# Performance work log

Measured on AMD Instinct MI355X. Metric: run time of the kernel, lower is better.

The kernel has to match this reference:

```python
import jax, jax.numpy as jnp
import numpy as np

BS, P, R, D = 32, 128, 16, 1024
RHO = 0.97
EPS = 1e-8


def unit_normalize(x):
    return x / jnp.maximum(jnp.linalg.norm(x, axis=-1, keepdims=True), EPS)


def setup_inputs() -> dict:
    key = jax.random.key(0)
    ks = jax.random.split(key, 12)
    scale = 1.0 / np.sqrt(D)
    return {
        "x_all": jax.random.normal(ks[0], (BS, P, D), jnp.float32),
        "h_all": jax.random.normal(ks[1], (BS, P, D), jnp.float32),
        "surprise_all": jax.random.uniform(ks[2], (BS, P, 1), jnp.float32) * 8.0,
        "reset_mask": jax.random.bernoulli(ks[3], 0.05, (BS, P)),
        "pm_K": unit_normalize(jax.random.normal(ks[4], (BS, R, D), jnp.float32)),
        "pm_V": unit_normalize(jax.random.normal(ks[5], (BS, R, D), jnp.float32)),
        "pm_a": jax.random.uniform(ks[6], (BS, R), jnp.float32),
        "elig_K0": jnp.zeros((BS, R, D), jnp.float32),
        "elig_V0": jnp.zeros((BS, R, D), jnp.float32),
        "W_k": jax.random.normal(ks[7], (D, D), jnp.float32) * scale,
        "b_k": jnp.zeros((D,), jnp.float32),
        "W_v": jax.random.normal(ks[8], (D, D), jnp.float32) * scale,
        "b_v": jnp.zeros((D,), jnp.float32),
    }


def reference(x_all, h_all, surprise_all, reset_mask, pm_K, pm_V, pm_a,
              elig_K0, elig_V0, W_k, b_k, W_v, b_v):
    # ---- apply_batch: read-only slot-memory readout over P tokens ----
    x_q = unit_normalize(x_all)                                  # [BS,P,D]
    scores = jnp.einsum('brd,bpd->bpr', pm_K, x_q)               # [BS,P,R]
    weighted = pm_a[:, None, :] * scores                         # [BS,P,R]
    y_pm = jnp.einsum('bpr,brd->bpd', weighted, pm_V)            # [BS,P,D]

    # ---- update_eligibility_batch: affine scan over P tokens ----
    k_cand = unit_normalize(jnp.einsum('bpd,de->bpe', x_all, W_k) + b_k)  # [BS,P,D]
    v_cand = jnp.einsum('bpd,de->bpe', h_all, W_v) + b_v                  # [BS,P,D]
    gate = jnp.clip(surprise_all[..., 0] / 5.0, 0.0, 1.0)                 # [BS,P]
    a_keep = RHO * (1.0 - reset_mask.astype(jnp.float32))                 # [BS,P]

    def step(carry, inp):
        eK, eV = carry                      # each [BS,R,D]
        k, v, g, a = inp                    # [BS,D],[BS,D],[BS],[BS]
        # b_t = gate * cand, broadcast across the R slots (matches torch expand)
        eK = a[:, None, None] * eK + (g[:, None] * k)[:, None, :]
        eV = a[:, None, None] * eV + (g[:, None] * v)[:, None, :]
        return (eK, eV), None

    xs = (jnp.swapaxes(k_cand, 0, 1), jnp.swapaxes(v_cand, 0, 1),
          gate.T, a_keep.T)                 # leading axis = P
    (elig_K, elig_V), _ = jax.lax.scan(step, (elig_K0, elig_V0), xs)

    return y_pm, elig_K, elig_V
```

## Files before the change

### kernel.cpp

```cpp
#include <hip/hip_runtime.h>
#include <cstdint>
#include <cstddef>

#define NB 32
#define NP 128
#define NR 16
#define ND 1024
#define RHOC 0.97f
#define EPSN 1e-8f

typedef short bf16x8 __attribute__((ext_vector_type(8)));
typedef float f32x4 __attribute__((ext_vector_type(4)));
typedef unsigned short u16x8 __attribute__((ext_vector_type(8)));
typedef unsigned short ushort_t;

__device__ inline ushort_t f2bf(float f) {
  unsigned u = __float_as_uint(f);
  unsigned r = (u + 0x7fffu + ((u >> 16) & 1u)) >> 16;
  return (ushort_t)r;
}
__device__ inline float bf2f(ushort_t v) {
  return __uint_as_float(((unsigned)v) << 16);
}
__device__ inline void gload16(const void* g, void* l) {
  __builtin_amdgcn_global_load_lds(
      (const __attribute__((address_space(1))) void*)g,
      (__attribute__((address_space(3))) void*)l, 16, 0, 0);
}

__global__ __launch_bounds__(256) void prep_kernel(
    const float* __restrict__ surprise, const void* __restrict__ mask,
    const float* __restrict__ x, const float* __restrict__ Wk,
    const float* __restrict__ pmK, const float* __restrict__ h,
    float* __restrict__ c, float* __restrict__ Abuf, float* __restrict__ csum,
    ushort_t* __restrict__ Xb, float* __restrict__ xnorm,
    ushort_t* __restrict__ WkT, ushort_t* __restrict__ pmKb,
    float* __restrict__ hbar) {
  __shared__ __align__(16) char smem[8448];
  int bid = blockIdx.x;
  int t = threadIdx.x;
  const unsigned char* mb = (const unsigned char*)mask;
  if (bid < NB) {
    float* a_sh = (float*)smem;
    float* suf  = a_sh + 128;
    float* redc = suf + 132;
    int*   isu8 = (int*)(redc + 128);
    int b = bid;
    if (t == 0) *isu8 = 0;
    __syncthreads();
    int v = 0;
    for (int i = t; i < NB * NP; i += 256)
      if ((i & 3) != 0 && mb[i] != 0) v = 1;
    if (v) *isu8 = 1;
    __syncthreads();
    int u8 = *isu8;
    if (t < NP) {
      int mv = u8 ? mb[b * NP + t] : ((const int*)mask)[b * NP + t];
      a_sh[t] = RHOC * (mv ? 0.f : 1.f);
    }
    __syncthreads();
    if (t == 0) {
      float p = 1.f;
      suf[NP] = 1.f;
      for (int s = NP - 1; s >= 0; --s) { p *= a_sh[s]; suf[s] = p; }
    }
    __syncthreads();
    if (t < NP) {
      float g = fminf(fmaxf(surprise[b * NP + t] * 0.2f, 0.f), 1.f);
      float cv = g * suf[t + 1];
      c[b * NP + t] = cv;
      redc[t] = cv;
    }
    __syncthreads();
    for (int off = 64; off > 0; off >>= 1) {
      if (t < off) redc[t] += redc[t + off];
      __syncthreads();
    }
    if (t == 0) { csum[b] = redc[0]; Abuf[b] = suf[0]; }
  } else if (bid < NB + 512) {
    int id = bid - NB;
    int b = id >> 4, dchunk = id & 15;
    float* asw = (float*)smem;
    float* suf = asw + 128;
    float* cs  = suf + 132;
    float* red = cs + 128;
    int* isu8  = (int*)(red + 256);
    if (t == 0) *isu8 = 0;
    __syncthreads();
    int v = 0;
    for (int i = t; i < NB * NP; i += 256)
      if ((i & 3) != 0 && mb[i] != 0) v = 1;
    if (v) *isu8 = 1;
    __syncthreads();
    int u8 = *isu8;
    if (t < NP) {
      int mv = u8 ? mb[b * NP + t] : ((const int*)mask)[b * NP + t];
      asw[t] = RHOC * (mv ? 0.f : 1.f);
    }
    __syncthreads();
    if (t == 0) {
      float p = 1.f;
      suf[NP] = 1.f;
      for (int s = NP - 1; s >= 0; --s) { p *= asw[s]; suf[s] = p; }
    }
    __syncthreads();
    if (t < NP) {
      float g = fminf(fmaxf(surprise[b * NP + t] * 0.2f, 0.f), 1.f);
      cs[t] = g * suf[t + 1];
    }
    __syncthreads();
    int dd = t & 63, sl = t >> 6;
    int d = dchunk * 64 + dd;
    const float* hb = h + ((size_t)b * NP + sl * 32) * ND + d;
    float acc = 0.f;
#pragma unroll
    for (int tt2 = 0; tt2 < 32; ++tt2)
      acc += cs[sl * 32 + tt2] * hb[(size_t)tt2 * ND];
    red[sl * 64 + dd] = acc;
    __syncthreads();
    if (sl == 0)
      hbar[(size_t)b * ND + d] = red[dd] + red[64 + dd] + red[128 + dd] + red[192 + dd];
  } else if (bid < NB + 512 + NB * NP) {
    int row = bid - (NB + 512);
    float* red = (float*)smem;
    float4 vv = *(const float4*)&x[(size_t)row * ND + t * 4];
    ushort4 o;
    o.x = f2bf(vv.x); o.y = f2bf(vv.y); o.z = f2bf(vv.z); o.w = f2bf(vv.w);
    *(ushort4*)&Xb[(size_t)row * ND + t * 4] = o;
    float ss = vv.x * vv.x + vv.y * vv.y + vv.z * vv.z + vv.w * vv.w;
#pragma unroll
    for (int off = 32; off > 0; off >>= 1) ss += __shfl_xor(ss, off);
    int wave = t >> 6, lane = t & 63;
    if (lane == 0) red[wave] = ss;
    __syncthreads();
    if (t == 0) xnorm[row] = sqrtf(red[0] + red[1] + red[2] + red[3]);
  } else if (bid < NB + 512 + NB * NP + 256) {
    int id2 = bid - (NB + 512 + NB * NP);
    ushort_t (*tt)[65] = (ushort_t(*)[65])smem;
    int k0 = (id2 >> 4) * 64, n0 = (id2 & 15) * 64;
#pragma unroll
    for (int i = 0; i < 16; ++i) {
      int r = i * 4 + (t >> 6), cc = t & 63;
      tt[r][cc] = f2bf(Wk[(size_t)(k0 + r) * ND + n0 + cc]);
    }
    __syncthreads();
#pragma unroll
    for (int i = 0; i < 16; ++i) {
      int r = i * 4 + (t >> 6), cc = t & 63;
      WkT[(size_t)(n0 + r) * ND + k0 + cc] = tt[cc][r];
    }
  } else {
    int id3 = bid - (NB + 512 + NB * NP + 256);
    size_t base = (size_t)id3 * 2048 + t * 8;
    float4 a = *(const float4*)&pmK[base];
    float4 bq = *(const float4*)&pmK[base + 4];
    u16x8 o;
    o[0] = f2bf(a.x); o[1] = f2bf(a.y); o[2] = f2bf(a.z); o[3] = f2bf(a.w);
    o[4] = f2bf(bq.x); o[5] = f2bf(bq.y); o[6] = f2bf(bq.z); o[7] = f2bf(bq.w);
    *(u16x8*)&pmKb[base] = o;
  }
}

__global__ __launch_bounds__(256, 3) void main_kernel(
    const ushort_t* __restrict__ Xb, const ushort_t* __restrict__ WkT,
    const float* __restrict__ bk, float* __restrict__ norms2p,
    const ushort_t* __restrict__ pmKb, const float* __restrict__ pmV,
    const float* __restrict__ pma, const float* __restrict__ xnorm,
    float* __restrict__ y) {
  __shared__ __align__(16) char smem[50176];
  int bid = blockIdx.x;
  int tid = threadIdx.x;
  if (bid < 512) {
    ushort_t* As = (ushort_t*)smem;
    ushort_t* Bs = As + 2 * 128 * 64;
    float* sred = (float*)(Bs + 2 * 64 * 64);
    int lane = tid & 63, wid = tid >> 6;
    int wr = wid >> 1, wc = wid & 1;
    int bm = bid & 31, bn = bid >> 5;
    int m0 = bm * 128, n0 = bn * 64;
    int lo = lane & 15, hi = lane >> 4;
    f32x4 acc[4][2] = {};

#define STAGE(buf, k0)                                                        \
  {                                                                           \
    _Pragma("unroll") for (int i = 0; i < 4; ++i) {                           \
      int sl = i * 256 + tid;                                                 \
      int r = sl >> 3, s = sl & 7;                                            \
      int gk = (k0) + ((s ^ (r & 7)) << 3);                                   \
      gload16(&Xb[(size_t)(m0 + r) * ND + gk],                                \
              &As[(size_t)(buf)*8192 + ((size_t)sl << 3)]);                   \
    }                                                                         \
    _Pragma("unroll") for (int i = 0; i < 2; ++i) {                           \
      int sl = i * 256 + tid;                                                 \
      int r = sl >> 3, s = sl & 7;                                            \
      int gk = (k0) + ((s ^ (r & 7)) << 3);                                   \
      gload16(&WkT[(size_t)(n0 + r) * ND + gk],                               \
              &Bs[(size_t)(buf)*4096 + ((size_t)sl << 3)]);                   \
    }                                                                         \
  }

    STAGE(0, 0);
    __syncthreads();
    int cur = 0;
    for (int t = 0; t < 16; ++t) {
      if (t < 15) STAGE(cur ^ 1, (t + 1) * 64);
      const ushort_t* Ab = As + cur * 8192;
      const ushort_t* Bb = Bs + cur * 4096;
#pragma unroll
      for (int ksl = 0; ksl < 2; ++ksl) {
        bf16x8 af[4], bfr[2];
#pragma unroll
        for (int mi = 0; mi < 4; ++mi) {
          int r = wr * 64 + mi * 16 + lo;
          int s = (ksl * 4 + hi) ^ (r & 7);
          af[mi] = *(const bf16x8*)&Ab[(r << 6) + (s << 3)];
        }
#pragma unroll
        for (int ni = 0; ni < 2; ++ni) {
          int r = wc * 32 + ni * 16 + lo;
          int s = (ksl * 4 + hi) ^ (r & 7);
          bfr[ni] = *(const bf16x8*)&Bb[(r << 6) + (s << 3)];
        }
#pragma unroll
        for (int mi = 0; mi < 4; ++mi)
#pragma unroll
          for (int ni = 0; ni < 2; ++ni)
            acc[mi][ni] = __builtin_amdgcn_mfma_f32_16x16x32_bf16(
                af[mi], bfr[ni], acc[mi][ni], 0, 0, 0);
      }
      __syncthreads();
      cur ^= 1;
    }
#undef STAGE
    float bkv[2];
#pragma unroll
    for (int ni = 0; ni < 2; ++ni) bkv[ni] = bk[n0 + wc * 32 + ni * 16 + lo];
#pragma unroll
    for (int mi = 0; mi < 4; ++mi) {
#pragma unroll
      for (int j = 0; j < 4; ++j) {
        float ss = 0.f;
#pragma unroll
        for (int ni = 0; ni < 2; ++ni) {
          float vv = acc[mi][ni][j] + bkv[ni];
          ss += vv * vv;
        }
        ss += __shfl_xor(ss, 1);
        ss += __shfl_xor(ss, 2);
        ss += __shfl_xor(ss, 4);
        ss += __shfl_xor(ss, 8);
        if (lo == 0) sred[wc * 128 + wr * 64 + mi * 16 + hi * 4 + j] = ss;
      }
    }
    __syncthreads();
    if (tid < 128)
      norms2p[(size_t)bn * (NB * NP) + m0 + tid] = sred[tid] + sred[128 + tid];
  } else {
    int id2 = bid - 512;
    int b = id2 >> 3, p0 = (id2 & 7) * 16;
    float* sredp = (float*)smem;
    float* wls = sredp + 4 * 16 * 17;
    int lane = tid & 63, wid = tid >> 6;
    int lo = lane & 15, hi = lane >> 4;
    float4 v[16];
#pragma unroll
    for (int r = 0; r < 16; ++r)
      v[r] = *(const float4*)&pmV[((size_t)(b * NR + r)) * ND + tid * 4];
    const ushort_t* xrow = &Xb[((size_t)(b * NP + p0 + lo)) * ND];
    const ushort_t* krow = &pmKb[((size_t)(b * NR + lo)) * ND];
    f32x4 sc = {};
#pragma unroll
    for (int ki = 0; ki < 8; ++ki) {
      int koff = (wid * 8 + ki) * 32 + hi * 8;
      bf16x8 af = *(const bf16x8*)&xrow[koff];
      bf16x8 bf = *(const bf16x8*)&krow[koff];
      sc = __builtin_amdgcn_mfma_f32_16x16x32_bf16(af, bf, sc, 0, 0, 0);
    }
#pragma unroll
    for (int j = 0; j < 4; ++j) sredp[(wid * 16 + hi * 4 + j) * 17 + lo] = sc[j];
    __syncthreads();
    {
      int p = tid >> 4, r = tid & 15;
      float s = sredp[(p)*17 + r] + sredp[(16 + p) * 17 + r] +
                sredp[(32 + p) * 17 + r] + sredp[(48 + p) * 17 + r];
      wls[p * 16 + r] = pma[b * NR + r] * s / fmaxf(xnorm[b * NP + p0 + p], EPSN);
    }
    __syncthreads();
#pragma unroll
    for (int p = 0; p < 16; ++p) {
      float4 a = {0.f, 0.f, 0.f, 0.f};
#pragma unroll
      for (int r = 0; r < 16; ++r) {
        float w = wls[p * 16 + r];
        a.x += w * v[r].x; a.y += w * v[r].y;
        a.z += w * v[r].z; a.w += w * v[r].w;
      }
      *(float4*)&y[((size_t)(b * NP + p0 + p)) * ND + tid * 4] = a;
    }
  }
}

__device__ __forceinline__ void eligout_body(
    int id, int tid, const float* __restrict__ src, const float* __restrict__ W,
    const float* __restrict__ bias, const float* __restrict__ coef,
    const float* __restrict__ e0, const float* __restrict__ Abuf,
    float* __restrict__ out, char* smemv) {
  int bg = id >> 4, dchunk = id & 15;
  int b0 = bg * 2;
  float* hs = (float*)smemv;
  float* red = hs + 2 * ND;
  for (int i = tid; i < 2 * ND; i += 256) {
    int bb = i >> 10, e = i & 1023;
    hs[bb * ND + e] = src[(size_t)(b0 + bb) * ND + e];
  }
  __syncthreads();
  int esl = tid >> 6, dd = tid & 63;
  int d = dchunk * 64 + dd;
  float a0 = 0.f, a1 = 0.f;
  const float* wcol = W + d;
#pragma unroll 8
  for (int ei = 0; ei < 256; ++ei) {
    int e = esl * 256 + ei;
    float w = wcol[(size_t)e * ND];
    a0 += hs[e] * w;
    a1 += hs[ND + e] * w;
  }
  red[(esl * 64 + dd) * 2 + 0] = a0;
  red[(esl * 64 + dd) * 2 + 1] = a1;
  __syncthreads();
  if (tid < 128) {
    int bb = tid >> 6, dd2 = tid & 63;
    int d2 = dchunk * 64 + dd2;
    float s = red[dd2 * 2 + bb] + red[(64 + dd2) * 2 + bb] +
              red[(128 + dd2) * 2 + bb] + red[(192 + dd2) * 2 + bb];
    int b = b0 + bb;
    s += coef[b] * bias[d2];
    float A = Abuf[b];
#pragma unroll
    for (int r = 0; r < NR; ++r) {
      size_t idx = ((size_t)(b * NR + r)) * ND + d2;
      out[idx] = A * e0[idx] + s;
    }
  }
}

__global__ __launch_bounds__(256) void d3_kernel(
    const float* __restrict__ hbar, const float* __restrict__ Wv,
    const float* __restrict__ bv, const float* __restrict__ csum,
    const float* __restrict__ eV0, const float* __restrict__ Abuf,
    float* __restrict__ outV,
    const ushort_t* __restrict__ Xb, const float* __restrict__ norms2p,
    const float* __restrict__ c, float* __restrict__ xbar,
    float* __restrict__ wsum) {
  __shared__ __align__(16) char smem[10240];
  int bid = blockIdx.x;
  int tid = threadIdx.x;
  if (bid < 256) {
    eligout_body(bid, tid, hbar, Wv, bv, csum, eV0, Abuf, outV, smem);
  } else {
    int id = bid - 256;
    float* wsh = (float*)smem;
    float* red = wsh + NP;
    int b = id >> 3;
    int dd = tid & 63, sl = tid >> 6;
    int d = (id & 7) * 128 + dd * 2;
    if (tid < NP) {
      float s = 0.f;
#pragma unroll
      for (int pc = 0; pc < 16; ++pc)
        s += norms2p[(size_t)pc * (NB * NP) + b * NP + tid];
      wsh[tid] = c[b * NP + tid] / fmaxf(sqrtf(s), EPSN);
    }
    __syncthreads();
    if ((id & 7) == 0 && tid == 0) {
      float s = 0.f;
      for (int t2 = 0; t2 < NP; ++t2) s += wsh[t2];
      wsum[b] = s;
    }
    const ushort_t* xb = Xb + ((size_t)b * NP + sl * 32) * ND + d;
    float ax = 0.f, ay = 0.f;
#pragma unroll
    for (int t2 = 0; t2 < 32; ++t2) {
      unsigned u = *(const unsigned*)&xb[(size_t)t2 * ND];
      float w = wsh[sl * 32 + t2];
      ax += w * bf2f((ushort_t)(u & 0xffffu));
      ay += w * bf2f((ushort_t)(u >> 16));
    }
    red[(sl * 64 + dd) * 2 + 0] = ax;
    red[(sl * 64 + dd) * 2 + 1] = ay;
    __syncthreads();
    if (sl == 0) {
      float2 o;
      o.x = red[dd * 2] + red[(64 + dd) * 2] + red[(128 + dd) * 2] + red[(192 + dd) * 2];
      o.y = red[dd * 2 + 1] + red[(64 + dd) * 2 + 1] + red[(128 + dd) * 2 + 1] +
            red[(192 + dd) * 2 + 1];
      *(float2*)&xbar[(size_t)b * ND + d] = o;
    }
  }
}

__global__ __launch_bounds__(256) void d4_kernel(
    const float* __restrict__ xbar, const float* __restrict__ Wk,
    const float* __restrict__ bk, const float* __restrict__ wsum,
    const float* __restrict__ eK0, const float* __restrict__ Abuf,
    float* __restrict__ outK) {
  __shared__ __align__(16) char smem[10240];
  eligout_body(blockIdx.x, threadIdx.x, xbar, Wk, bk, wsum, eK0, Abuf, outK, smem);
}

extern "C" void kernel_launch(void* const* d_in, const int* in_sizes, int n_in,
                              void* d_out, int out_size, void* d_ws, size_t ws_size,
                              hipStream_t stream) {
  (void)in_sizes; (void)n_in; (void)out_size; (void)ws_size;
  const float* x_all    = (const float*)d_in[0];
  const float* h_all    = (const float*)d_in[1];
  const float* surprise = (const float*)d_in[2];
  const void*  mask     = d_in[3];
  const float* pmK      = (const float*)d_in[4];
  const float* pmV      = (const float*)d_in[5];
  const float* pma      = (const float*)d_in[6];
  const float* eK0      = (const float*)d_in[7];
  const float* eV0      = (const float*)d_in[8];
  const float* Wk       = (const float*)d_in[9];
  const float* bk       = (const float*)d_in[10];
  const float* Wv       = (const float*)d_in[11];
  const float* bv       = (const float*)d_in[12];

  float* y    = (float*)d_out;
  float* outK = y + (size_t)NB * NP * ND;
  float* outV = outK + (size_t)NB * NR * ND;

  char* w = (char*)d_ws;
  float* c        = (float*)w; w += NB * NP * 4;
  float* Abuf     = (float*)w; w += 256;
  float* csum     = (float*)w; w += 256;
  float* wsum     = (float*)w; w += 256;
  float* hbar     = (float*)w; w += NB * ND * 4;
  float* xbar     = (float*)w; w += NB * ND * 4;
  float* norms2p  = (float*)w; w += (size_t)16 * NB * NP * 4;
  float* xnorm    = (float*)w; w += NB * NP * 4;
  ushort_t* WkT   = (ushort_t*)w; w += (size_t)ND * ND * 2;
  ushort_t* pmKb  = (ushort_t*)w; w += (size_t)NB * NR * ND * 2;
  ushort_t* Xb    = (ushort_t*)w; w += (size_t)NB * NP * ND * 2;

  prep_kernel<<<NB + 512 + NB * NP + 256 + 256, 256, 0, stream>>>(
      surprise, mask, x_all, Wk, pmK, h_all, c, Abuf, csum, Xb, xnorm, WkT,
      pmKb, hbar);
  main_kernel<<<512 + 256, 256, 0, stream>>>(Xb, WkT, bk, norms2p, pmKb, pmV,
                                             pma, xnorm, y);
  d3_kernel<<<256 + 256, 256, 0, stream>>>(hbar, Wv, bv, csum, eV0, Abuf, outV,
                                           Xb, norms2p, c, xbar, wsum);
  d4_kernel<<<256, 256, 0, stream>>>(xbar, Wk, bk, wsum, eK0, Abuf, outK);
}
```

Baseline: 66.26 us.

## Fold slot readout into prep kernel and regroup kernels around GEMM

The y readout now runs in the first kernel. It reads fp32 x and pm_K directly, converts them to bf16 in registers and computes the row norms inline, so the separate xnorm and pmKb buffers and their conversion blocks are gone. The x-to-bf16 conversion now uses 1024 blocks of 4096 elements instead of one block per row. The K-projection GEMM now runs in the same launch as the V eligibility output, and its shared-memory staging drops from double to single buffering, which roughly halves LDS use but loses load/compute overlap. The xbar reduction becomes its own smaller kernel.

```diff
diff --git a/kernel.cpp b/kernel.cpp
--- a/kernel.cpp
+++ b/kernel.cpp
@@ -11,7 +11,6 @@
 
 typedef short bf16x8 __attribute__((ext_vector_type(8)));
 typedef float f32x4 __attribute__((ext_vector_type(4)));
-typedef unsigned short u16x8 __attribute__((ext_vector_type(8)));
 typedef unsigned short ushort_t;
 
 __device__ inline ushort_t f2bf(float f) {
@@ -22,30 +21,88 @@
 __device__ inline float bf2f(ushort_t v) {
   return __uint_as_float(((unsigned)v) << 16);
 }
+__device__ inline bf16x8 cvt8(float4 a, float4 b) {
+  union { bf16x8 v; ushort_t u[8]; } o;
+  o.u[0] = f2bf(a.x); o.u[1] = f2bf(a.y); o.u[2] = f2bf(a.z); o.u[3] = f2bf(a.w);
+  o.u[4] = f2bf(b.x); o.u[5] = f2bf(b.y); o.u[6] = f2bf(b.z); o.u[7] = f2bf(b.w);
+  return o.v;
+}
 __device__ inline void gload16(const void* g, void* l) {
   __builtin_amdgcn_global_load_lds(
       (const __attribute__((address_space(1))) void*)g,
       (__attribute__((address_space(3))) void*)l, 16, 0, 0);
 }
 
-__global__ __launch_bounds__(256) void prep_kernel(
+__global__ __launch_bounds__(256) void d1_kernel(
     const float* __restrict__ surprise, const void* __restrict__ mask,
     const float* __restrict__ x, const float* __restrict__ Wk,
-    const float* __restrict__ pmK, const float* __restrict__ h,
+    const float* __restrict__ pmK, const float* __restrict__ pmV,
+    const float* __restrict__ pma, const float* __restrict__ h,
     float* __restrict__ c, float* __restrict__ Abuf, float* __restrict__ csum,
-    ushort_t* __restrict__ Xb, float* __restrict__ xnorm,
-    ushort_t* __restrict__ WkT, ushort_t* __restrict__ pmKb,
-    float* __restrict__ hbar) {
+    ushort_t* __restrict__ Xb, ushort_t* __restrict__ WkT,
+    float* __restrict__ hbar, float* __restrict__ y) {
   __shared__ __align__(16) char smem[8448];
   int bid = blockIdx.x;
   int t = threadIdx.x;
   const unsigned char* mb = (const unsigned char*)mask;
-  if (bid < NB) {
+  if (bid < 256) {
+    int b = bid >> 3, p0 = (bid & 7) * 16;
+    float* sredp = (float*)smem;
+    float* wls = sredp + 4 * 16 * 17;
+    float* rowssq = wls + 256;
+    int lane = t & 63, wid = t >> 6;
+    int lo = lane & 15, hi = lane >> 4;
+    float4 v[16];
+#pragma unroll
+    for (int r = 0; r < 16; ++r)
+      v[r] = *(const float4*)&pmV[((size_t)(b * NR + r)) * ND + t * 4];
+    const float* xrow = &x[((size_t)(b * NP + p0 + lo)) * ND];
+    const float* krow = &pmK[((size_t)(b * NR + lo)) * ND];
+    f32x4 sc = {};
+    float ssq = 0.f;
+#pragma unroll
+    for (int ki = 0; ki < 8; ++ki) {
+      int koff = (wid * 8 + ki) * 32 + hi * 8;
+      float4 xa = *(const float4*)&xrow[koff];
+      float4 xc = *(const float4*)&xrow[koff + 4];
+      ssq += xa.x * xa.x + xa.y * xa.y + xa.z * xa.z + xa.w * xa.w +
+             xc.x * xc.x + xc.y * xc.y + xc.z * xc.z + xc.w * xc.w;
+      float4 ka = *(const float4*)&krow[koff];
+      float4 kc = *(const float4*)&krow[koff + 4];
+      sc = __builtin_amdgcn_mfma_f32_16x16x32_bf16(cvt8(xa, xc), cvt8(ka, kc),
+                                                   sc, 0, 0, 0);
+    }
+    ssq += __shfl_xor(ssq, 16);
+    ssq += __shfl_xor(ssq, 32);
+    if (hi == 0) rowssq[wid * 16 + lo] = ssq;
+#pragma unroll
+    for (int j = 0; j < 4; ++j) sredp[(wid * 16 + hi * 4 + j) * 17 + lo] = sc[j];
+    __syncthreads();
+    {
+      int p = t >> 4, r = t & 15;
+      float s = sredp[p * 17 + r] + sredp[(16 + p) * 17 + r] +
+                sredp[(32 + p) * 17 + r] + sredp[(48 + p) * 17 + r];
+      float nrm = sqrtf(rowssq[p] + rowssq[16 + p] + rowssq[32 + p] + rowssq[48 + p]);
+      wls[p * 16 + r] = pma[b * NR + r] * s / fmaxf(nrm, EPSN);
+    }
+    __syncthreads();
+#pragma unroll
+    for (int p = 0; p < 16; ++p) {
+      float4 a = {0.f, 0.f, 0.f, 0.f};
+#pragma unroll
+      for (int r = 0; r < 16; ++r) {
+        float w = wls[p * 16 + r];
+        a.x += w * v[r].x; a.y += w * v[r].y;
+        a.z += w * v[r].z; a.w += w * v[r].w;
+      }
+      *(float4*)&y[((size_t)(b * NP + p0 + p)) * ND + t * 4] = a;
+    }
+  } else if (bid < 256 + NB) {
+    int b = bid - 256;
     float* a_sh = (float*)smem;
     float* suf  = a_sh + 128;
     float* redc = suf + 132;
     int*   isu8 = (int*)(redc + 128);
-    int b = bid;
     if (t == 0) *isu8 = 0;
     __syncthreads();
     int v = 0;
@@ -77,8 +134,8 @@
       __syncthreads();
     }
     if (t == 0) { csum[b] = redc[0]; Abuf[b] = suf[0]; }
-  } else if (bid < NB + 512) {
-    int id = bid - NB;
+  } else if (bid < 256 + NB + 512) {
+    int id = bid - (256 + NB);
     int b = id >> 4, dchunk = id & 15;
     float* asw = (float*)smem;
     float* suf = asw + 128;
@@ -120,22 +177,8 @@
     __syncthreads();
     if (sl == 0)
       hbar[(size_t)b * ND + d] = red[dd] + red[64 + dd] + red[128 + dd] + red[192 + dd];
-  } else if (bid < NB + 512 + NB * NP) {
-    int row = bid - (NB + 512);
-    float* red = (float*)smem;
-    float4 vv = *(const float4*)&x[(size_t)row * ND + t * 4];
-    ushort4 o;
-    o.x = f2bf(vv.x); o.y = f2bf(vv.y); o.z = f2bf(vv.z); o.w = f2bf(vv.w);
-    *(ushort4*)&Xb[(size_t)row * ND + t * 4] = o;
-    float ss = vv.x * vv.x + vv.y * vv.y + vv.z * vv.z + vv.w * vv.w;
-#pragma unroll
-    for (int off = 32; off > 0; off >>= 1) ss += __shfl_xor(ss, off);
-    int wave = t >> 6, lane = t & 63;
-    if (lane == 0) red[wave] = ss;
-    __syncthreads();
-    if (t == 0) xnorm[row] = sqrtf(red[0] + red[1] + red[2] + red[3]);
-  } else if (bid < NB + 512 + NB * NP + 256) {
-    int id2 = bid - (NB + 512 + NB * NP);
+  } else if (bid < 256 + NB + 512 + 256) {
+    int id2 = bid - (256 + NB + 512);
     ushort_t (*tt)[65] = (ushort_t(*)[65])smem;
     int k0 = (id2 >> 4) * 64, n0 = (id2 & 15) * 64;
 #pragma unroll
@@ -150,152 +193,15 @@
       WkT[(size_t)(n0 + r) * ND + k0 + cc] = tt[cc][r];
     }
   } else {
-    int id3 = bid - (NB + 512 + NB * NP + 256);
-    size_t base = (size_t)id3 * 2048 + t * 8;
-    float4 a = *(const float4*)&pmK[base];
-    float4 bq = *(const float4*)&pmK[base + 4];
-    u16x8 o;
-    o[0] = f2bf(a.x); o[1] = f2bf(a.y); o[2] = f2bf(a.z); o[3] = f2bf(a.w);
-    o[4] = f2bf(bq.x); o[5] = f2bf(bq.y); o[6] = f2bf(bq.z); o[7] = f2bf(bq.w);
-    *(u16x8*)&pmKb[base] = o;
-  }
-}
-
-__global__ __launch_bounds__(256, 3) void main_kernel(
-    const ushort_t* __restrict__ Xb, const ushort_t* __restrict__ WkT,
-    const float* __restrict__ bk, float* __restrict__ norms2p,
-    const ushort_t* __restrict__ pmKb, const float* __restrict__ pmV,
-    const float* __restrict__ pma, const float* __restrict__ xnorm,
-    float* __restrict__ y) {
-  __shared__ __align__(16) char smem[50176];
-  int bid = blockIdx.x;
-  int tid = threadIdx.x;
-  if (bid < 512) {
-    ushort_t* As = (ushort_t*)smem;
-    ushort_t* Bs = As + 2 * 128 * 64;
-    float* sred = (float*)(Bs + 2 * 64 * 64);
-    int lane = tid & 63, wid = tid >> 6;
-    int wr = wid >> 1, wc = wid & 1;
-    int bm = bid & 31, bn = bid >> 5;
-    int m0 = bm * 128, n0 = bn * 64;
-    int lo = lane & 15, hi = lane >> 4;
-    f32x4 acc[4][2] = {};
-
-#define STAGE(buf, k0)                                                        \
-  {                                                                           \
-    _Pragma("unroll") for (int i = 0; i < 4; ++i) {                           \
-      int sl = i * 256 + tid;                                                 \
-      int r = sl >> 3, s = sl & 7;                                            \
-      int gk = (k0) + ((s ^ (r & 7)) << 3);                                   \
-      gload16(&Xb[(size_t)(m0 + r) * ND + gk],                                \
-              &As[(size_t)(buf)*8192 + ((size_t)sl << 3)]);                   \
-    }                                                                         \
-    _Pragma("unroll") for (int i = 0; i < 2; ++i) {                           \
-      int sl = i * 256 + tid;                                                 \
-      int r = sl >> 3, s = sl & 7;                                            \
-      int gk = (k0) + ((s ^ (r & 7)) << 3);                                   \
-      gload16(&WkT[(size_t)(n0 + r) * ND + gk],                               \
-              &Bs[(size_t)(buf)*4096 + ((size_t)sl << 3)]);                   \
-    }                                                                         \
-  }
-
-    STAGE(0, 0);
-    __syncthreads();
-    int cur = 0;
-    for (int t = 0; t < 16; ++t) {
-      if (t < 15) STAGE(cur ^ 1, (t + 1) * 64);
-      const ushort_t* Ab = As + cur * 8192;
-      const ushort_t* Bb = Bs + cur * 4096;
-#pragma unroll
-      for (int ksl = 0; ksl < 2; ++ksl) {
-        bf16x8 af[4], bfr[2];
-#pragma unroll
-        for (int mi = 0; mi < 4; ++mi) {
-          int r = wr * 64 + mi * 16 + lo;
-          int s = (ksl * 4 + hi) ^ (r & 7);
-          af[mi] = *(const bf16x8*)&Ab[(r << 6) + (s << 3)];
-        }
-#pragma unroll
-        for (int ni = 0; ni < 2; ++ni) {
-          int r = wc * 32 + ni * 16 + lo;
-          int s = (ksl * 4 + hi) ^ (r & 7);
-          bfr[ni] = *(const bf16x8*)&Bb[(r << 6) + (s << 3)];
-        }
-#pragma unroll
-        for (int mi = 0; mi < 4; ++mi)
-#pragma unroll
-          for (int ni = 0; ni < 2; ++ni)
-            acc[mi][ni] = __builtin_amdgcn_mfma_f32_16x16x32_bf16(
-                af[mi], bfr[ni], acc[mi][ni], 0, 0, 0);
-      }
-      __syncthreads();
-      cur ^= 1;
-    }
-#undef STAGE
-    float bkv[2];
-#pragma unroll
-    for (int ni = 0; ni < 2; ++ni) bkv[ni] = bk[n0 + wc * 32 + ni * 16 + lo];
-#pragma unroll
-    for (int mi = 0; mi < 4; ++mi) {
-#pragma unroll
-      for (int j = 0; j < 4; ++j) {
-        float ss = 0.f;
-#pragma unroll
-        for (int ni = 0; ni < 2; ++ni) {
-          float vv = acc[mi][ni][j] + bkv[ni];
-          ss += vv * vv;
-        }
-        ss += __shfl_xor(ss, 1);
-        ss += __shfl_xor(ss, 2);
-        ss += __shfl_xor(ss, 4);
-        ss += __shfl_xor(ss, 8);
-        if (lo == 0) sred[wc * 128 + wr * 64 + mi * 16 + hi * 4 + j] = ss;
-      }
-    }
-    __syncthreads();
-    if (tid < 128)
-      norms2p[(size_t)bn * (NB * NP) + m0 + tid] = sred[tid] + sred[128 + tid];
-  } else {
-    int id2 = bid - 512;
-    int b = id2 >> 3, p0 = (id2 & 7) * 16;
-    float* sredp = (float*)smem;
-    float* wls = sredp + 4 * 16 * 17;
-    int lane = tid & 63, wid = tid >> 6;
-    int lo = lane & 15, hi = lane >> 4;
-    float4 v[16];
-#pragma unroll
-    for (int r = 0; r < 16; ++r)
-      v[r] = *(const float4*)&pmV[((size_t)(b * NR + r)) * ND + tid * 4];
-    const ushort_t* xrow = &Xb[((size_t)(b * NP + p0 + lo)) * ND];
-    const ushort_t* krow = &pmKb[((size_t)(b * NR + lo)) * ND];
-    f32x4 sc = {};
-#pragma unroll
-    for (int ki = 0; ki < 8; ++ki) {
-      int koff = (wid * 8 + ki) * 32 + hi * 8;
-      bf16x8 af = *(const bf16x8*)&xrow[koff];
-      bf16x8 bf = *(const bf16x8*)&krow[koff];
-      sc = __builtin_amdgcn_mfma_f32_16x16x32_bf16(af, bf, sc, 0, 0, 0);
-    }
-#pragma unroll
-    for (int j = 0; j < 4; ++j) sredp[(wid * 16 + hi * 4 + j) * 17 + lo] = sc[j];
-    __syncthreads();
-    {
-      int p = tid >> 4, r = tid & 15;
-      float s = sredp[(p)*17 + r] + sredp[(16 + p) * 17 + r] +
-                sredp[(32 + p) * 17 + r] + sredp[(48 + p) * 17 + r];
-      wls[p * 16 + r] = pma[b * NR + r] * s / fmaxf(xnorm[b * NP + p0 + p], EPSN);
-    }
-    __syncthreads();
-#pragma unroll
-    for (int p = 0; p < 16; ++p) {
-      float4 a = {0.f, 0.f, 0.f, 0.f};
-#pragma unroll
-      for (int r = 0; r < 16; ++r) {
-        float w = wls[p * 16 + r];
-        a.x += w * v[r].x; a.y += w * v[r].y;
-        a.z += w * v[r].z; a.w += w * v[r].w;
-      }
-      *(float4*)&y[((size_t)(b * NP + p0 + p)) * ND + tid * 4] = a;
+    int id3 = bid - (256 + NB + 512 + 256);
+    size_t base = (size_t)id3 * 4096;
+#pragma unroll
+    for (int i = 0; i < 4; ++i) {
+      size_t idx = base + i * 1024 + t * 4;
+      float4 vv = *(const float4*)&x[idx];
+      ushort4 o;
+      o.x = f2bf(vv.x); o.y = f2bf(vv.y); o.z = f2bf(vv.z); o.w = f2bf(vv.w);
+      *(ushort4*)&Xb[idx] = o;
     }
   }
 }
@@ -344,58 +250,137 @@
   }
 }
 
-__global__ __launch_bounds__(256) void d3_kernel(
+__global__ __launch_bounds__(256) void d2_kernel(
+    const ushort_t* __restrict__ Xb, const ushort_t* __restrict__ WkT,
+    const float* __restrict__ bk, float* __restrict__ norms2p,
     const float* __restrict__ hbar, const float* __restrict__ Wv,
     const float* __restrict__ bv, const float* __restrict__ csum,
     const float* __restrict__ eV0, const float* __restrict__ Abuf,
-    float* __restrict__ outV,
+    float* __restrict__ outV) {
+  __shared__ __align__(16) char smem[25600];
+  int bid = blockIdx.x;
+  int tid = threadIdx.x;
+  if (bid < 512) {
+    ushort_t* As = (ushort_t*)smem;
+    ushort_t* Bs = As + 128 * 64;
+    float* sred = (float*)(Bs + 64 * 64);
+    int lane = tid & 63, wid = tid >> 6;
+    int wr = wid >> 1, wc = wid & 1;
+    int bm = bid & 31, bn = bid >> 5;
+    int m0 = bm * 128, n0 = bn * 64;
+    int lo = lane & 15, hi = lane >> 4;
+    f32x4 acc[4][2] = {};
+    for (int k0 = 0; k0 < ND; k0 += 64) {
+#pragma unroll
+      for (int i = 0; i < 4; ++i) {
+        int sl = i * 256 + tid;
+        int r = sl >> 3, s = sl & 7;
+        int gk = k0 + ((s ^ (r & 7)) << 3);
+        gload16(&Xb[(size_t)(m0 + r) * ND + gk], &As[sl << 3]);
+      }
+#pragma unroll
+      for (int i = 0; i < 2; ++i) {
+        int sl = i * 256 + tid;
+        int r = sl >> 3, s = sl & 7;
+        int gk = k0 + ((s ^ (r & 7)) << 3);
+        gload16(&WkT[(size_t)(n0 + r) * ND + gk], &Bs[sl << 3]);
+      }
+      __syncthreads();
+#pragma unroll
+      for (int ksl = 0; ksl < 2; ++ksl) {
+        bf16x8 af[4], bfr[2];
+#pragma unroll
+        for (int mi = 0; mi < 4; ++mi) {
+          int r = wr * 64 + mi * 16 + lo;
+          int s = (ksl * 4 + hi) ^ (r & 7);
+          af[mi] = *(const bf16x8*)&As[(r << 6) + (s << 3)];
+        }
+#pragma unroll
+        for (int ni = 0; ni < 2; ++ni) {
+          int r = wc * 32 + ni * 16 + lo;
+          int s = (ksl * 4 + hi) ^ (r & 7);
+          bfr[ni] = *(const bf16x8*)&Bs[(r << 6) + (s << 3)];
+        }
+#pragma unroll
+        for (int mi = 0; mi < 4; ++mi)
+#pragma unroll
+          for (int ni = 0; ni < 2; ++ni)
+            acc[mi][ni] = __builtin_amdgcn_mfma_f32_16x16x32_bf16(
+                af[mi], bfr[ni], acc[mi][ni], 0, 0, 0);
+      }
+      __syncthreads();
+    }
+    float bkv[2];
+#pragma unroll
+    for (int ni = 0; ni < 2; ++ni) bkv[ni] = bk[n0 + wc * 32 + ni * 16 + lo];
+#pragma unroll
+    for (int mi = 0; mi < 4; ++mi) {
+#pragma unroll
+      for (int j = 0; j < 4; ++j) {
+        float ss = 0.f;
+#pragma unroll
+        for (int ni = 0; ni < 2; ++ni) {
+          float vv = acc[mi][ni][j] + bkv[ni];
+          ss += vv * vv;
+        }
+        ss += __shfl_xor(ss, 1);
+        ss += __shfl_xor(ss, 2);
+        ss += __shfl_xor(ss, 4);
+        ss += __shfl_xor(ss, 8);
+        if (lo == 0) sred[wc * 128 + wr * 64 + mi * 16 + hi * 4 + j] = ss;
+      }
+    }
+    __syncthreads();
+    if (tid < 128)
+      norms2p[(size_t)bn * (NB * NP) + m0 + tid] = sred[tid] + sred[128 + tid];
+  } else {
+    eligout_body(bid - 512, tid, hbar, Wv, bv, csum, eV0, Abuf, outV, smem);
+  }
+}
+
+__global__ __launch_bounds__(256) void d3_kernel(
     const ushort_t* __restrict__ Xb, const float* __restrict__ norms2p,
     const float* __restrict__ c, float* __restrict__ xbar,
     float* __restrict__ wsum) {
-  __shared__ __align__(16) char smem[10240];
+  __shared__ __align__(16) char smem[2560];
   int bid = blockIdx.x;
   int tid = threadIdx.x;
-  if (bid < 256) {
-    eligout_body(bid, tid, hbar, Wv, bv, csum, eV0, Abuf, outV, smem);
-  } else {
-    int id = bid - 256;
-    float* wsh = (float*)smem;
-    float* red = wsh + NP;
-    int b = id >> 3;
-    int dd = tid & 63, sl = tid >> 6;
-    int d = (id & 7) * 128 + dd * 2;
-    if (tid < NP) {
-      float s = 0.f;
-#pragma unroll
-      for (int pc = 0; pc < 16; ++pc)
-        s += norms2p[(size_t)pc * (NB * NP) + b * NP + tid];
-      wsh[tid] = c[b * NP + tid] / fmaxf(sqrtf(s), EPSN);
-    }
-    __syncthreads();
-    if ((id & 7) == 0 && tid == 0) {
-      float s = 0.f;
-      for (int t2 = 0; t2 < NP; ++t2) s += wsh[t2];
-      wsum[b] = s;
-    }
-    const ushort_t* xb = Xb + ((size_t)b * NP + sl * 32) * ND + d;
-    float ax = 0.f, ay = 0.f;
-#pragma unroll
-    for (int t2 = 0; t2 < 32; ++t2) {
-      unsigned u = *(const unsigned*)&xb[(size_t)t2 * ND];
-      float w = wsh[sl * 32 + t2];
-      ax += w * bf2f((ushort_t)(u & 0xffffu));
-      ay += w * bf2f((ushort_t)(u >> 16));
-    }
-    red[(sl * 64 + dd) * 2 + 0] = ax;
-    red[(sl * 64 + dd) * 2 + 1] = ay;
-    __syncthreads();
-    if (sl == 0) {
-      float2 o;
-      o.x = red[dd * 2] + red[(64 + dd) * 2] + red[(128 + dd) * 2] + red[(192 + dd) * 2];
-      o.y = red[dd * 2 + 1] + red[(64 + dd) * 2 + 1] + red[(128 + dd) * 2 + 1] +
-            red[(192 + dd) * 2 + 1];
-      *(float2*)&xbar[(size_t)b * ND + d] = o;
-    }
+  float* wsh = (float*)smem;
+  float* red = wsh + NP;
+  int b = bid >> 3;
+  int dd = tid & 63, sl = tid >> 6;
+  int d = (bid & 7) * 128 + dd * 2;
+  if (tid < NP) {
+    float s = 0.f;
+#pragma unroll
+    for (int pc = 0; pc < 16; ++pc)
+      s += norms2p[(size_t)pc * (NB * NP) + b * NP + tid];
+    wsh[tid] = c[b * NP + tid] / fmaxf(sqrtf(s), EPSN);
+  }
+  __syncthreads();
+  if ((bid & 7) == 0 && tid == 0) {
+    float s = 0.f;
+    for (int t2 = 0; t2 < NP; ++t2) s += wsh[t2];
+    wsum[b] = s;
+  }
+  const ushort_t* xb = Xb + ((size_t)b * NP + sl * 32) * ND + d;
+  float ax = 0.f, ay = 0.f;
+#pragma unroll
+  for (int t2 = 0; t2 < 32; ++t2) {
+    unsigned u = *(const unsigned*)&xb[(size_t)t2 * ND];
+    float w = wsh[sl * 32 + t2];
+    ax += w * bf2f((ushort_t)(u & 0xffffu));
+    ay += w * bf2f((ushort_t)(u >> 16));
+  }
+  red[(sl * 64 + dd) * 2 + 0] = ax;
+  red[(sl * 64 + dd) * 2 + 1] = ay;
+  __syncthreads();
+  if (sl == 0) {
+    float2 o;
+    o.x = red[dd * 2] + red[(64 + dd) * 2] + red[(128 + dd) * 2] + red[(192 + dd) * 2];
+    o.y = red[dd * 2 + 1] + red[(64 + dd) * 2 + 1] + red[(128 + dd) * 2 + 1] +
+          red[(192 + dd) * 2 + 1];
+    *(float2*)&xbar[(size_t)b * ND + d] = o;
   }
 }
 
@@ -438,17 +423,14 @@
   float* hbar     = (float*)w; w += NB * ND * 4;
   float* xbar     = (float*)w; w += NB * ND * 4;
   float* norms2p  = (float*)w; w += (size_t)16 * NB * NP * 4;
-  float* xnorm    = (float*)w; w += NB * NP * 4;
   ushort_t* WkT   = (ushort_t*)w; w += (size_t)ND * ND * 2;
-  ushort_t* pmKb  = (ushort_t*)w; w += (size_t)NB * NR * ND * 2;
   ushort_t* Xb    = (ushort_t*)w; w += (size_t)NB * NP * ND * 2;
 
-  prep_kernel<<<NB + 512 + NB * NP + 256 + 256, 256, 0, stream>>>(
-      surprise, mask, x_all, Wk, pmK, h_all, c, Abuf, csum, Xb, xnorm, WkT,
-      pmKb, hbar);
-  main_kernel<<<512 + 256, 256, 0, stream>>>(Xb, WkT, bk, norms2p, pmKb, pmV,
-                                             pma, xnorm, y);
-  d3_kernel<<<256 + 256, 256, 0, stream>>>(hbar, Wv, bv, csum, eV0, Abuf, outV,
-                                           Xb, norms2p, c, xbar, wsum);
+  d1_kernel<<<256 + NB + 512 + 256 + 1024, 256, 0, stream>>>(
+      surprise, mask, x_all, Wk, pmK, pmV, pma, h_all, c, Abuf, csum, Xb, WkT,
+      hbar, y);
+  d2_kernel<<<512 + 256, 256, 0, stream>>>(Xb, WkT, bk, norms2p, hbar, Wv, bv,
+                                           csum, eV0, Abuf, outV);
+  d3_kernel<<<256, 256, 0, stream>>>(Xb, norms2p, c, xbar, wsum);
   d4_kernel<<<256, 256, 0, stream>>>(xbar, Wk, bk, wsum, eK0, Abuf, outK);
 }
```

New measurement: 61.57 us. 1.08x faster.
